# Optimization experiments

Measured on AMD Instinct MI355X. Metric: run time of the kernel, lower is better.

The kernel has to match this reference:

```python
import jax, jax.numpy as jnp
import numpy as np

NUM_POINTS = 2_000_000
N = 2_000_000

# SH constants (standard real spherical harmonics, as in gaussian-splatting)
C0 = 0.28209479177387814
C1 = 0.4886025119029199
C2 = (1.0925484305920792, -1.0925484305920792, 0.31539156525252005,
      -1.0925484305920792, 0.5462742152960396)
C3 = (-0.5900435899266435, 2.890611442640554, -0.4570457994644658,
      0.3731763325901154, -0.4570457994644658, 1.445305721320277,
      -0.5900435899266435)


def sh_basis_deg3(dirs):
    # dirs: [N,3] unit vectors -> basis [N,16]
    x, y, z = dirs[:, 0], dirs[:, 1], dirs[:, 2]
    xx, yy, zz = x * x, y * y, z * z
    xy, yz, xz = x * y, y * z, x * z
    one = jnp.ones_like(x)
    return jnp.stack([
        C0 * one,
        -C1 * y, C1 * z, -C1 * x,
        C2[0] * xy, C2[1] * yz, C2[2] * (2.0 * zz - xx - yy),
        C2[3] * xz, C2[4] * (xx - yy),
        C3[0] * y * (3.0 * xx - yy), C3[1] * xy * z,
        C3[2] * y * (4.0 * zz - xx - yy),
        C3[3] * z * (2.0 * zz - 3.0 * xx - 3.0 * yy),
        C3[4] * x * (4.0 * zz - xx - yy),
        C3[5] * z * (xx - yy), C3[6] * x * (xx - yy),
    ], axis=-1)


def setup_inputs() -> dict:
    key = jax.random.key(0)
    ks = jax.random.split(key, 8)
    return {
        "positions": jax.random.normal(ks[0], (N, 3), jnp.float32),
        "indexes": jax.random.randint(ks[1], (N,), 0, NUM_POINTS, jnp.int64)
            if jax.config.jax_enable_x64 else
            jax.random.randint(ks[1], (N,), 0, NUM_POINTS, jnp.int32),
        "cam_pos": jax.random.normal(ks[2], (3,), jnp.float32),
        "glo_feature": jax.random.normal(ks[3], (1, 16), jnp.float32),
        "base_sh": jax.random.normal(ks[4], (NUM_POINTS, 3, 1), jnp.float32),
        "higher_sh": jnp.zeros((NUM_POINTS, 3, 15), jnp.float32)
            + 0.01 * jax.random.normal(ks[5], (NUM_POINTS, 3, 15), jnp.float32),
        "w1": jax.random.normal(ks[6], (16, 32), jnp.float32) * (1.0 / np.sqrt(16)),
        "b1": jnp.zeros((32,), jnp.float32),
        "ln_w": jnp.ones((32,), jnp.float32),
        "ln_b": jnp.zeros((32,), jnp.float32),
        "w2": jax.random.normal(ks[7], (32, 12), jnp.float32) * (1.0 / np.sqrt(32)),
        "b2": jnp.zeros((12,), jnp.float32),
    }


def mlp(glo, w1, b1, ln_w, ln_b, w2, b2, out_scale=1e-12):
    h = glo @ w1 + b1                      # [1,32]
    mu = jnp.mean(h, axis=-1, keepdims=True)
    var = jnp.mean((h - mu) ** 2, axis=-1, keepdims=True)
    h = (h - mu) * jax.lax.rsqrt(var + 1e-5) * ln_w + ln_b
    h = jax.nn.relu(h)
    return (h @ w2 + b2) * out_scale       # [1,12]


def reference(positions, indexes, cam_pos, glo_feature, base_sh, higher_sh,
              w1, b1, ln_w, ln_b, w2, b2):
    sh_features = jnp.concatenate([base_sh, higher_sh], axis=2)  # [P,3,16]
    sh = sh_features[indexes]                                    # gather [N,3,16]
    dirs = positions - cam_pos
    dirs = dirs / jnp.linalg.norm(dirs, axis=-1, keepdims=True)
    basis = sh_basis_deg3(dirs)                                  # [N,16]
    colors = jnp.einsum('nck,nk->nc', sh, basis) + 0.5           # [N,3]
    colors4 = jnp.concatenate([colors, jnp.ones_like(colors[:, :1])], axis=1)  # [N,4]
    affine_res = mlp(glo_feature, w1, b1, ln_w, ln_b, w2, b2).reshape(1, 3, 4)
    affine = affine_res + jnp.eye(3, 4, dtype=jnp.float32)[None]  # [1,3,4]
    out = jnp.einsum('nj,ij->ni', colors4, affine[0])             # [N,3]
    return jnp.clip(out, 0.0, 1.0), jnp.mean(jnp.abs(affine_res))
```

## Files before the change

### kernel.cpp

```cpp
#include <hip/hip_runtime.h>
#include <math.h>


__global__ __launch_bounds__(64) void mlp_prologue_kernel(
    const float* __restrict__ glo,
    const float* __restrict__ w1,
    const float* __restrict__ b1,
    const float* __restrict__ ln_w,
    const float* __restrict__ ln_b,
    const float* __restrict__ w2,
    const float* __restrict__ b2,
    float* __restrict__ affine_out,
    float* __restrict__ mean_out)
{
    __shared__ float hsh[32];
    __shared__ float ssh[12];
    int t = threadIdx.x;

    float h = 0.f;
    if (t < 32) {
        h = b1[t];
        #pragma unroll
        for (int k = 0; k < 16; ++k) h += glo[k] * w1[k * 32 + t];
    }
    float s = h;
    #pragma unroll
    for (int off = 32; off > 0; off >>= 1) s += __shfl_down(s, off);
    float mu = __shfl(s, 0) * (1.f / 32.f);

    float d = (t < 32) ? (h - mu) : 0.f;
    float v2 = d * d;
    #pragma unroll
    for (int off = 32; off > 0; off >>= 1) v2 += __shfl_down(v2, off);
    float var = __shfl(v2, 0) * (1.f / 32.f);
    float inv = rsqrtf(var + 1e-5f);

    if (t < 32) {
        float v = (h - mu) * inv * ln_w[t] + ln_b[t];
        hsh[t] = v > 0.f ? v : 0.f;
    }
    __syncthreads();
    if (t < 12) {
        float s2 = b2[t];
        #pragma unroll
        for (int j = 0; j < 32; ++j) s2 += hsh[j] * w2[j * 12 + t];
        s2 *= 1e-12f;
        ssh[t] = fabsf(s2);
        float e = ((t & 3) == (t >> 2)) ? 1.f : 0.f;
        affine_out[t] = s2 + e;
    }
    __syncthreads();
    if (t == 0) {
        float sa = 0.f;
        #pragma unroll
        for (int i = 0; i < 12; ++i) sa += ssh[i];
        *mean_out = sa * (1.f / 12.f);
    }
}

__global__ __launch_bounds__(256) void transfer_sh_kernel(
    const float* __restrict__ positions,
    const int*   __restrict__ indexes,
    const float* __restrict__ cam_pos,
    const float* __restrict__ base_sh,
    const float* __restrict__ higher_sh,
    const float* __restrict__ affine,
    float* __restrict__ out,
    int n)
{
    int i = blockIdx.x * blockDim.x + threadIdx.x;
    if (i >= n) return;

    float px = positions[3 * i + 0] - cam_pos[0];
    float py = positions[3 * i + 1] - cam_pos[1];
    float pz = positions[3 * i + 2] - cam_pos[2];
    float rn = rsqrtf(px * px + py * py + pz * pz);
    float x = px * rn, y = py * rn, z = pz * rn;

    float xx = x * x, yy = y * y, zz = z * z;
    float xy = x * y, yz = y * z, xz = x * z;

    float b[16];
    b[1]  = -0.4886025119029199f * y;
    b[2]  =  0.4886025119029199f * z;
    b[3]  = -0.4886025119029199f * x;
    b[4]  =  1.0925484305920792f * xy;
    b[5]  = -1.0925484305920792f * yz;
    b[6]  =  0.31539156525252005f * (2.f * zz - xx - yy);
    b[7]  = -1.0925484305920792f * xz;
    b[8]  =  0.5462742152960396f * (xx - yy);
    b[9]  = -0.5900435899266435f * y * (3.f * xx - yy);
    b[10] =  2.890611442640554f  * xy * z;
    b[11] = -0.4570457994644658f * y * (4.f * zz - xx - yy);
    b[12] =  0.3731763325901154f * z * (2.f * zz - 3.f * xx - 3.f * yy);
    b[13] = -0.4570457994644658f * x * (4.f * zz - xx - yy);
    b[14] =  1.445305721320277f  * z * (xx - yy);
    b[15] = -0.5900435899266435f * x * (xx - yy);

    unsigned idx = (unsigned)indexes[i];

    float a0 = base_sh[3 * idx + 0];
    float a1 = base_sh[3 * idx + 1];
    float a2 = base_sh[3 * idx + 2];
    const float C0 = 0.28209479177387814f;
    float c0 = a0 * C0 + 0.5f;
    float c1 = a1 * C0 + 0.5f;
    float c2 = a2 * C0 + 0.5f;

    unsigned fo = 45u * idx;
    const float4* W = (const float4*)(higher_sh + (fo & ~3u));
    float4 v[12];
    #pragma unroll
    for (int q = 0; q < 12; ++q) v[q] = W[q];
    float Wf[48];
    #pragma unroll
    for (int q = 0; q < 12; ++q) {
        Wf[4 * q + 0] = v[q].x; Wf[4 * q + 1] = v[q].y;
        Wf[4 * q + 2] = v[q].z; Wf[4 * q + 3] = v[q].w;
    }

#define ACC(M)                                      \
    {                                               \
        _Pragma("unroll")                           \
        for (int k = 0; k < 15; ++k) {              \
            c0 += Wf[(M) + k]      * b[k + 1];      \
            c1 += Wf[(M) + 15 + k] * b[k + 1];      \
            c2 += Wf[(M) + 30 + k] * b[k + 1];      \
        }                                           \
    }
    switch (fo & 3u) {
        case 0: ACC(0) break;
        case 1: ACC(1) break;
        case 2: ACC(2) break;
        default: ACC(3) break;
    }
#undef ACC

    #pragma unroll
    for (int r = 0; r < 3; ++r) {
        float vv = c0 * affine[4 * r + 0] + c1 * affine[4 * r + 1] +
                   c2 * affine[4 * r + 2] + affine[4 * r + 3];
        vv = fminf(fmaxf(vv, 0.f), 1.f);
        out[3 * i + r] = vv;
    }
}

extern "C" void kernel_launch(void* const* d_in, const int* in_sizes, int n_in,
                              void* d_out, int out_size, void* d_ws, size_t ws_size,
                              hipStream_t stream) {
    const float* positions = (const float*)d_in[0];
    const int*   indexes   = (const int*)d_in[1];
    const float* cam_pos   = (const float*)d_in[2];
    const float* glo       = (const float*)d_in[3];
    const float* base_sh   = (const float*)d_in[4];
    const float* higher_sh = (const float*)d_in[5];
    const float* w1        = (const float*)d_in[6];
    const float* b1        = (const float*)d_in[7];
    const float* ln_w      = (const float*)d_in[8];
    const float* ln_b      = (const float*)d_in[9];
    const float* w2        = (const float*)d_in[10];
    const float* b2        = (const float*)d_in[11];

    float* out    = (float*)d_out;
    float* affine = (float*)d_ws;

    int n = in_sizes[0] / 3;
    float* mean_out = out + (out_size - 1);

    mlp_prologue_kernel<<<1, 64, 0, stream>>>(glo, w1, b1, ln_w, ln_b, w2, b2,
                                              affine, mean_out);

    int block = 256;
    int grid = (n + block - 1) / block;
    transfer_sh_kernel<<<grid, block, 0, stream>>>(positions, indexes, cam_pos,
                                                   base_sh, higher_sh, affine,
                                                   out, n);
}
```

Measured before the change: 579.9 us.

## Fuse MLP prologue into gather kernel and issue gathers before per-block MLP

Removes the separate single-block MLP kernel launch. Every block now recomputes the tiny affine MLP into shared memory, and block 0 writes the mean. The indexed SH gathers and position loads are issued before the MLP and its barriers, so memory latency can overlap that compute. Loads and stores of the streamed data use nontemporal hints. The cost is redundant MLP work and two extra __syncthreads in every block, plus higher register pressure from holding the gathered data across the barriers.

```diff
diff --git a/kernel.cpp b/kernel.cpp
--- a/kernel.cpp
+++ b/kernel.cpp
@@ -2,42 +2,69 @@
 #include <math.h>
 
 
-__global__ __launch_bounds__(64) void mlp_prologue_kernel(
+__global__ __launch_bounds__(256) void transfer_sh_fused(
+    const float* __restrict__ positions,
+    const int*   __restrict__ indexes,
+    const float* __restrict__ cam_pos,
     const float* __restrict__ glo,
+    const float* __restrict__ base_sh,
+    const float* __restrict__ higher_sh,
     const float* __restrict__ w1,
     const float* __restrict__ b1,
     const float* __restrict__ ln_w,
     const float* __restrict__ ln_b,
     const float* __restrict__ w2,
     const float* __restrict__ b2,
-    float* __restrict__ affine_out,
-    float* __restrict__ mean_out)
+    float* __restrict__ out,
+    float* __restrict__ mean_out,
+    int n)
 {
+    __shared__ float aff[12];
     __shared__ float hsh[32];
     __shared__ float ssh[12];
-    int t = threadIdx.x;
 
-    float h = 0.f;
-    if (t < 32) {
-        h = b1[t];
+    const int t = threadIdx.x;
+    const int i = blockIdx.x * 256 + t;
+    const bool active = (i < n);
+    const int ie = active ? i : (n - 1);
+
+    unsigned idx = (unsigned)__builtin_nontemporal_load(indexes + ie);
+
+    float px = __builtin_nontemporal_load(positions + 3 * ie + 0);
+    float py = __builtin_nontemporal_load(positions + 3 * ie + 1);
+    float pz = __builtin_nontemporal_load(positions + 3 * ie + 2);
+
+    float a0 = base_sh[3 * idx + 0];
+    float a1 = base_sh[3 * idx + 1];
+    float a2 = base_sh[3 * idx + 2];
+
+    unsigned fo = 45u * idx;
+    const float4* W = (const float4*)(higher_sh + (fo & ~3u));
+    float4 v[12];
+    #pragma unroll
+    for (int q = 0; q < 12; ++q) v[q] = W[q];
+
+    if (t < 64) {
+        float h = 0.f;
+        if (t < 32) {
+            h = b1[t];
+            #pragma unroll
+            for (int k = 0; k < 16; ++k) h += glo[k] * w1[k * 32 + t];
+        }
+        float s = h;
         #pragma unroll
-        for (int k = 0; k < 16; ++k) h += glo[k] * w1[k * 32 + t];
-    }
-    float s = h;
-    #pragma unroll
-    for (int off = 32; off > 0; off >>= 1) s += __shfl_down(s, off);
-    float mu = __shfl(s, 0) * (1.f / 32.f);
-
-    float d = (t < 32) ? (h - mu) : 0.f;
-    float v2 = d * d;
-    #pragma unroll
-    for (int off = 32; off > 0; off >>= 1) v2 += __shfl_down(v2, off);
-    float var = __shfl(v2, 0) * (1.f / 32.f);
-    float inv = rsqrtf(var + 1e-5f);
-
-    if (t < 32) {
-        float v = (h - mu) * inv * ln_w[t] + ln_b[t];
-        hsh[t] = v > 0.f ? v : 0.f;
+        for (int off = 32; off > 0; off >>= 1) s += __shfl_down(s, off);
+        float mu = __shfl(s, 0) * (1.f / 32.f);
+        float d = (t < 32) ? (h - mu) : 0.f;
+        float v2 = d * d;
+        #pragma unroll
+        for (int off = 32; off > 0; off >>= 1) v2 += __shfl_down(v2, off);
+        float var = __shfl(v2, 0) * (1.f / 32.f);
+        float inv = rsqrtf(var + 1e-5f);
+        if (t < 32) {
+            float hv = (h - mu) * inv * ln_w[t] + ln_b[t];
+            hsh[t] = hv > 0.f ? hv : 0.f;
+        }
     }
     __syncthreads();
     if (t < 12) {
@@ -47,35 +74,21 @@
         s2 *= 1e-12f;
         ssh[t] = fabsf(s2);
         float e = ((t & 3) == (t >> 2)) ? 1.f : 0.f;
-        affine_out[t] = s2 + e;
+        aff[t] = s2 + e;
     }
     __syncthreads();
-    if (t == 0) {
+    if (blockIdx.x == 0 && t == 0) {
         float sa = 0.f;
         #pragma unroll
-        for (int i = 0; i < 12; ++i) sa += ssh[i];
+        for (int q2 = 0; q2 < 12; ++q2) sa += ssh[q2];
         *mean_out = sa * (1.f / 12.f);
     }
-}
 
-__global__ __launch_bounds__(256) void transfer_sh_kernel(
-    const float* __restrict__ positions,
-    const int*   __restrict__ indexes,
-    const float* __restrict__ cam_pos,
-    const float* __restrict__ base_sh,
-    const float* __restrict__ higher_sh,
-    const float* __restrict__ affine,
-    float* __restrict__ out,
-    int n)
-{
-    int i = blockIdx.x * blockDim.x + threadIdx.x;
-    if (i >= n) return;
-
-    float px = positions[3 * i + 0] - cam_pos[0];
-    float py = positions[3 * i + 1] - cam_pos[1];
-    float pz = positions[3 * i + 2] - cam_pos[2];
-    float rn = rsqrtf(px * px + py * py + pz * pz);
-    float x = px * rn, y = py * rn, z = pz * rn;
+    float dx = px - cam_pos[0];
+    float dy = py - cam_pos[1];
+    float dz = pz - cam_pos[2];
+    float rn = rsqrtf(dx * dx + dy * dy + dz * dz);
+    float x = dx * rn, y = dy * rn, z = dz * rn;
 
     float xx = x * x, yy = y * y, zz = z * z;
     float xy = x * y, yz = y * z, xz = x * z;
@@ -97,21 +110,11 @@
     b[14] =  1.445305721320277f  * z * (xx - yy);
     b[15] = -0.5900435899266435f * x * (xx - yy);
 
-    unsigned idx = (unsigned)indexes[i];
-
-    float a0 = base_sh[3 * idx + 0];
-    float a1 = base_sh[3 * idx + 1];
-    float a2 = base_sh[3 * idx + 2];
     const float C0 = 0.28209479177387814f;
     float c0 = a0 * C0 + 0.5f;
     float c1 = a1 * C0 + 0.5f;
     float c2 = a2 * C0 + 0.5f;
 
-    unsigned fo = 45u * idx;
-    const float4* W = (const float4*)(higher_sh + (fo & ~3u));
-    float4 v[12];
-    #pragma unroll
-    for (int q = 0; q < 12; ++q) v[q] = W[q];
     float Wf[48];
     #pragma unroll
     for (int q = 0; q < 12; ++q) {
@@ -136,12 +139,14 @@
     }
 #undef ACC
 
-    #pragma unroll
-    for (int r = 0; r < 3; ++r) {
-        float vv = c0 * affine[4 * r + 0] + c1 * affine[4 * r + 1] +
-                   c2 * affine[4 * r + 2] + affine[4 * r + 3];
-        vv = fminf(fmaxf(vv, 0.f), 1.f);
-        out[3 * i + r] = vv;
+    if (active) {
+        #pragma unroll
+        for (int r = 0; r < 3; ++r) {
+            float vv = c0 * aff[4 * r + 0] + c1 * aff[4 * r + 1] +
+                       c2 * aff[4 * r + 2] + aff[4 * r + 3];
+            vv = fminf(fmaxf(vv, 0.f), 1.f);
+            __builtin_nontemporal_store(vv, out + 3 * i + r);
+        }
     }
 }
 
@@ -161,18 +166,14 @@
     const float* w2        = (const float*)d_in[10];
     const float* b2        = (const float*)d_in[11];
 
-    float* out    = (float*)d_out;
-    float* affine = (float*)d_ws;
+    float* out = (float*)d_out;
 
     int n = in_sizes[0] / 3;
     float* mean_out = out + (out_size - 1);
 
-    mlp_prologue_kernel<<<1, 64, 0, stream>>>(glo, w1, b1, ln_w, ln_b, w2, b2,
-                                              affine, mean_out);
-
     int block = 256;
     int grid = (n + block - 1) / block;
-    transfer_sh_kernel<<<grid, block, 0, stream>>>(positions, indexes, cam_pos,
-                                                   base_sh, higher_sh, affine,
-                                                   out, n);
+    transfer_sh_fused<<<grid, block, 0, stream>>>(
+        positions, indexes, cam_pos, glo, base_sh, higher_sh,
+        w1, b1, ln_w, ln_b, w2, b2, out, mean_out, n);
 }
```

Result: no change. 569.5 us, median of 2 (-1.8%).
